# Kernel optimization log

Hardware: AMD Instinct MI355X
Metric: run time of the kernel (lower is better)

## Reference

```python
import jax, jax.numpy as jnp
import numpy as np

B, N, D, F = 4096, 64, 64, 4096
KP_DIM = N * (N + 1) // 2  # 2080
# static row-major triu/tril index lists (matches torch.masked_select ordering)
_TRIU_I, _TRIU_J = (np.array(a) for a in np.triu_indices(N, 0))
_TRIL_I, _TRIL_J = (np.array(a) for a in np.tril_indices(N, 0))


def setup_inputs() -> dict:
    key = jax.random.key(0)
    k1, k2, k3, k4 = jax.random.split(key, 4)
    feature_emb = jax.random.normal(k1, (B, N, D), dtype=jnp.float32)
    # xavier_normal for [D, D]
    std = float(np.sqrt(2.0 / (D + D)))
    kp_W = jax.random.normal(k2, (D, D), dtype=jnp.float32) * std
    # nn.Linear weights are [out_features, in_features]
    bound = float(1.0 / np.sqrt(KP_DIM))
    W_triu = jax.random.uniform(k3, (F, KP_DIM), dtype=jnp.float32, minval=-bound, maxval=bound)
    W_tril = jax.random.uniform(k4, (F, KP_DIM), dtype=jnp.float32, minval=-bound, maxval=bound)
    return {"feature_emb": feature_emb, "kp_W": kp_W, "W_triu": W_triu, "W_tril": W_tril}


def reference(feature_emb, kp_W, W_triu, W_tril):
    # embs_kp[b,i,j] = e[b,i,:] @ kp_W @ e[b,j,:]  -> [B, N, N]
    embs_kp = jnp.einsum("bnd,de,bme->bnm", feature_emb, kp_W, feature_emb)
    triu = embs_kp[:, _TRIU_I, _TRIU_J]  # [B, kp_dim], row-major order
    tril = embs_kp[:, _TRIL_I, _TRIL_J]  # [B, kp_dim]
    embs_flatten = feature_emb.reshape(feature_emb.shape[0], -1)  # [B, N*D]
    view_1 = triu @ W_triu.T  # [B, F]
    view_2 = tril @ W_tril.T  # [B, F]
    return (embs_flatten, view_1, view_2)
```

## Files before the change

### kernel.cpp

```cpp
#include <hip/hip_runtime.h>

typedef __bf16 bf16x8 __attribute__((ext_vector_type(8)));
typedef float f32x4 __attribute__((ext_vector_type(4)));
typedef unsigned short u16x4 __attribute__((ext_vector_type(4)));
typedef unsigned short u16x8 __attribute__((ext_vector_type(8)));

#define KP 2112
#define NT 33

__device__ __forceinline__ unsigned short f2bf(float f) {
  unsigned int u = __builtin_bit_cast(unsigned int, f);
  u += 0x7FFFu + ((u >> 16) & 1u);
  return (unsigned short)(u >> 16);
}

__device__ __forceinline__ bf16x8 ld_frag(const unsigned short* p) {
  return __builtin_bit_cast(bf16x8, *(const u16x8*)p);
}

#define MFMA16(a, b, c) __builtin_amdgcn_mfma_f32_16x16x32_bf16((a), (b), (c), 0, 0, 0)

__device__ __forceinline__ void cp16(const void* g, void* l) {
  __builtin_amdgcn_global_load_lds(
      (const __attribute__((address_space(1))) unsigned int*)g,
      (__attribute__((address_space(3))) unsigned int*)l, 16, 0, 0);
}

__device__ __forceinline__ void barrier_sync() {
  asm volatile("s_waitcnt lgkmcnt(0)" ::: "memory");
  __builtin_amdgcn_s_barrier();
  __builtin_amdgcn_sched_barrier(0);
}

#define VMWAIT(N) asm volatile("s_waitcnt vmcnt(" #N ")" ::: "memory")

__global__ __launch_bounds__(256) void cvt_pad(
    const float* __restrict__ inu, const float* __restrict__ inl,
    unsigned short* __restrict__ outu, unsigned short* __restrict__ outl) {
  const float* in = blockIdx.y ? inl : inu;
  unsigned short* out = blockIdx.y ? outl : outu;
  const int row = blockIdx.x;
  const float* src = in + (size_t)row * 2080;
  unsigned short* dst = out + (size_t)row * KP;
  for (int c = threadIdx.x; c < 528; c += 256) {
    u16x4 o = {0, 0, 0, 0};
    if (c < 520) {
      float4 v = *(const float4*)(src + c * 4);
      o[0] = f2bf(v.x); o[1] = f2bf(v.y); o[2] = f2bf(v.z); o[3] = f2bf(v.w);
    }
    ((u16x4*)dst)[c] = o;
  }
}

__global__ __launch_bounds__(256) void prep_wt(const float* __restrict__ W,
                                               unsigned short* __restrict__ Wt) {
  const int o = blockIdx.x * 256 + threadIdx.x;
  const int c = o >> 6, d = o & 63;
  Wt[o] = f2bf(W[d * 64 + c]);
}

__device__ __forceinline__ void emit_tri(const unsigned short* __restrict__ sK,
                                         unsigned short* __restrict__ dst,
                                         bool upper, int tid) {
#pragma unroll
  for (int jj = 0; jj < 2; ++jj) {
    if (jj == 1 && tid >= 8) break;
    const int p0 = (jj == 0) ? tid * 8 : 2048 + tid * 8;
    int i, j;
    if (upper) {
      float s = sqrtf(4160.25f - 2.0f * (float)p0);
      i = (int)(64.5f - s);
      if (i < 0) i = 0;
      if (i > 63) i = 63;
      while (i > 0 && i * (129 - i) / 2 > p0) --i;
      while (i < 63 && (i + 1) * (128 - i) / 2 <= p0) ++i;
      j = i + (p0 - i * (129 - i) / 2);
    } else {
      float s = sqrtf(8.0f * (float)p0 + 1.0f);
      i = (int)((s - 1.0f) * 0.5f);
      if (i < 0) i = 0;
      if (i > 63) i = 63;
      while (i > 0 && i * (i + 1) / 2 > p0) --i;
      while (i < 63 && (i + 1) * (i + 2) / 2 <= p0) ++i;
      j = p0 - i * (i + 1) / 2;
    }
    u16x8 o;
#pragma unroll
    for (int e = 0; e < 8; ++e) {
      const int p = p0 + e;
      o[e] = (p < 2080 && i < 64) ? sK[i * 64 + j] : (unsigned short)0;
      if (upper) { if (++j > 63) { ++i; j = i; } }
      else       { if (++j > i)  { ++i; j = 0; } }
    }
    *(u16x8*)(dst + p0) = o;
  }
}

__global__ __launch_bounds__(256) void batch_kp(
    const float* __restrict__ E,
    const unsigned short* __restrict__ Wt,
    float* __restrict__ out0,
    unsigned short* __restrict__ triu,
    unsigned short* __restrict__ tril)
{
  __shared__ __align__(16) unsigned short sE[64 * 64];
  __shared__ __align__(16) unsigned short sWt[64 * 64];
  __shared__ __align__(16) unsigned short sT[64 * 64];

  const int b = blockIdx.x;
  const int tid = threadIdx.x;
  const float* Eb = E + (size_t)b * 4096;
  float* o0 = out0 + (size_t)b * 4096;

  cp16(Wt + tid * 8, sWt + tid * 8);
  cp16(Wt + 2048 + tid * 8, sWt + 2048 + tid * 8);

#pragma unroll
  for (int it = 0; it < 4; ++it) {
    const int flat = it * 1024 + tid * 4;
    float4 v = *(const float4*)(Eb + flat);
    *(float4*)(o0 + flat) = v;
    u16x4 e;
    e[0] = f2bf(v.x); e[1] = f2bf(v.y); e[2] = f2bf(v.z); e[3] = f2bf(v.w);
    *(u16x4*)(sE + flat) = e;
  }
  __syncthreads();

  const int lane = tid & 63, w = tid >> 6;
  const int fr = lane & 15;
  const int fk = (lane >> 4) << 3;
  const int qr = (lane >> 4) << 2;

#pragma unroll
  for (int ct = 0; ct < 4; ++ct) {
    f32x4 acc = {0.f, 0.f, 0.f, 0.f};
#pragma unroll
    for (int k2 = 0; k2 < 2; ++k2) {
      bf16x8 a = ld_frag(sE + (w * 16 + fr) * 64 + k2 * 32 + fk);
      bf16x8 bb = ld_frag(sWt + (ct * 16 + fr) * 64 + k2 * 32 + fk);
      acc = MFMA16(a, bb, acc);
    }
#pragma unroll
    for (int r = 0; r < 4; ++r)
      sT[(w * 16 + qr + r) * 64 + ct * 16 + fr] = f2bf(acc[r]);
  }
  __syncthreads();

  unsigned short* sK = sWt;
#pragma unroll
  for (int ct = 0; ct < 4; ++ct) {
    f32x4 acc = {0.f, 0.f, 0.f, 0.f};
#pragma unroll
    for (int k2 = 0; k2 < 2; ++k2) {
      bf16x8 a = ld_frag(sT + (w * 16 + fr) * 64 + k2 * 32 + fk);
      bf16x8 bb = ld_frag(sE + (ct * 16 + fr) * 64 + k2 * 32 + fk);
      acc = MFMA16(a, bb, acc);
    }
#pragma unroll
    for (int r = 0; r < 4; ++r)
      sK[(w * 16 + qr + r) * 64 + ct * 16 + fr] = f2bf(acc[r]);
  }
  __syncthreads();

  emit_tri(sK, triu + (size_t)b * KP, true, tid);
  emit_tri(sK, tril + (size_t)b * KP, false, tid);
}

__global__ __launch_bounds__(512, 2) void gemm_views(
    const unsigned short* __restrict__ triu, const unsigned short* __restrict__ tril,
    const unsigned short* __restrict__ Wu, const unsigned short* __restrict__ Wl,
    float* __restrict__ dout)
{
  __shared__ __align__(16) unsigned short lds[65536];

  const int z = blockIdx.z;
  const unsigned short* Ag = z ? tril : triu;
  const unsigned short* Bg = z ? Wl : Wu;
  float* C = dout + (size_t)16777216 * (size_t)(1 + z);

  const int tid = threadIdx.x;
  const int lane = tid & 63, wv = tid >> 6;
  const int m0 = blockIdx.y << 8, n0 = blockIdx.x << 8;

  const int lr = lane >> 3;
  const int cuch = (lane & 7) ^ lr;
  const int rA = wv * 8 + lr;
  const int rB = (wv & 3) * 8 + (wv >> 2) * 64 + lr;
  const unsigned short* gA = Ag + (size_t)(m0 + rA) * KP + cuch * 8;
  const unsigned short* gB = Bg + (size_t)(n0 + rB) * KP + cuch * 8;
  const int dA = tid * 8;
  const int dB = (wv & 3) * 512 + (wv >> 2) * 4096 + lane * 8;

  const int fr = lane & 15, fq = lane >> 4;
  const int rowA0 = (wv >> 2) * 128 + fr;
  const int rowB0 = (wv & 3) * 64 + fr;

  f32x4 acc[8][4] = {};
  bf16x8 aA_[4], aB_[4], bA_[4], bB_[4];

#define STAGE_A(B_, KT, OFF) do { \
    cp16(gA + (size_t)(OFF) * KP + (KT) * 64, lds + (B_) * 32768 + (OFF) * 64 + dA); \
    cp16(gA + (size_t)((OFF) + 128) * KP + (KT) * 64, \
         lds + (B_) * 32768 + ((OFF) + 128) * 64 + dA); \
  } while (0)
#define STAGE_B(B_, KT, OFF) do { \
    cp16(gB + (size_t)(OFF) * KP + (KT) * 64, \
         lds + (B_) * 32768 + 16384 + (OFF) * 64 + dB); \
    cp16(gB + (size_t)((OFF) + 128) * KP + (KT) * 64, \
         lds + (B_) * 32768 + 16384 + ((OFF) + 128) * 64 + dB); \
  } while (0)
#define LDA(S, B_, MH, KH) do { _Pragma("unroll") \
    for (int mt = 0; mt < 4; ++mt) \
      S[mt] = ld_frag(lds + (B_) * 32768 + (rowA0 + (MH) * 64 + mt * 16) * 64 + \
                      ((((KH) * 4 + fq) ^ (fr & 7)) * 8)); \
  } while (0)
#define LDB(S, B_, KH) do { _Pragma("unroll") \
    for (int nt = 0; nt < 4; ++nt) \
      S[nt] = ld_frag(lds + (B_) * 32768 + 16384 + (rowB0 + nt * 16) * 64 + \
                      ((((KH) * 4 + fq) ^ (fr & 7)) * 8)); \
  } while (0)
#define PH_MFMA(AS, BS, MH) do { \
    __builtin_amdgcn_s_setprio(1); \
    _Pragma("unroll") for (int mt = 0; mt < 4; ++mt) \
    _Pragma("unroll") for (int nt = 0; nt < 4; ++nt) \
      acc[(MH) * 4 + mt][nt] = MFMA16(AS[mt], BS[nt], acc[(MH) * 4 + mt][nt]); \
    __builtin_amdgcn_s_setprio(0); \
  } while (0)

  STAGE_A(0, 0, 0);
  STAGE_B(0, 0, 0);
  STAGE_B(0, 0, 32);
  STAGE_A(0, 0, 64);
  STAGE_B(1, 1, 0);
  STAGE_B(1, 1, 32);
  STAGE_A(1, 1, 0);
  VMWAIT(6);
  barrier_sync();
  LDA(aB_, 0, 0, 0);
  LDB(bA_, 0, 0);

  for (int t = 0; t < NT; ++t) {
    const int cb = t & 1, nb = cb ^ 1;
    const int t1 = (t + 1 < NT) ? t + 1 : NT - 1;
    const int t2 = (t + 2 < NT) ? t + 2 : NT - 1;
    LDA(aA_, cb, 1, 0);
    STAGE_A(nb, t1, 64);
    PH_MFMA(aB_, bA_, 0);
    barrier_sync();
    LDA(aB_, cb, 1, 1);
    LDB(bB_, cb, 1);
    PH_MFMA(aA_, bA_, 1);
    barrier_sync();
    LDA(aA_, cb, 0, 1);
    STAGE_B(cb, t2, 0);
    PH_MFMA(aB_, bB_, 1);
    VMWAIT(4);
    barrier_sync();
    LDA(aB_, nb, 0, 0);
    LDB(bA_, nb, 0);
    STAGE_B(cb, t2, 32);
    STAGE_A(cb, t2, 0);
    PH_MFMA(aA_, bB_, 0);
    VMWAIT(6);
    barrier_sync();
  }

  const int qr = fq << 2;
  const int crow = m0 + (wv >> 2) * 128 + qr;
  const int ccol = n0 + (wv & 3) * 64 + fr;
#pragma unroll
  for (int mt = 0; mt < 8; ++mt)
#pragma unroll
    for (int nt = 0; nt < 4; ++nt) {
      float* cp = C + (size_t)(crow + mt * 16) * 4096 + (ccol + nt * 16);
#pragma unroll
      for (int r = 0; r < 4; ++r) cp[(size_t)r * 4096] = acc[mt][nt][r];
    }
#undef STAGE_A
#undef STAGE_B
#undef LDA
#undef LDB
#undef PH_MFMA
}

extern "C" void kernel_launch(void* const* d_in, const int* in_sizes, int n_in,
                              void* d_out, int out_size, void* d_ws, size_t ws_size,
                              hipStream_t stream) {
  const float* feat  = (const float*)d_in[0];
  const float* kpW   = (const float*)d_in[1];
  const float* Wtriu = (const float*)d_in[2];
  const float* Wtril = (const float*)d_in[3];
  float* out = (float*)d_out;

  const size_t per = (size_t)4096 * KP;
  unsigned short* triu_bf = (unsigned short*)d_ws;
  unsigned short* tril_bf = triu_bf + per;
  unsigned short* Wu_bf   = tril_bf + per;
  unsigned short* Wl_bf   = Wu_bf + per;
  unsigned short* Wt_bf   = Wl_bf + per;

  cvt_pad<<<dim3(4096, 2), dim3(256), 0, stream>>>(Wtriu, Wtril, Wu_bf, Wl_bf);
  prep_wt<<<dim3(16), dim3(256), 0, stream>>>(kpW, Wt_bf);
  batch_kp<<<dim3(4096), dim3(256), 0, stream>>>(feat, Wt_bf, out, triu_bf, tril_bf);
  gemm_views<<<dim3(16, 16, 2), dim3(512), 0, stream>>>(triu_bf, tril_bf, Wu_bf, Wl_bf, out);
}
```

Before: 428.4 us.

## Fuse prep kernels into one launch and restructure GEMM barrier pipeline

Merges the weight fp32->bf16 conversion, the kp_W transpose, and the per-batch bilinear kernel into a single launch. Extra blocks handle the weight conversion and each batch block transposes kp_W itself, which removes two kernel launches and the Wt workspace round trip. The GEMM main loop is also rescheduled: LDS fragment loads now sit before a barrier that waits on lgkmcnt, with a separate closing barrier, rather than being prefetched across phases. This trades some register-level load/MFMA overlap for fewer live fragment registers, and adds redundant kp_W reads plus scattered LDS stores in every batch block.

```diff
diff --git a/kernel.cpp b/kernel.cpp
--- a/kernel.cpp
+++ b/kernel.cpp
@@ -26,38 +26,18 @@
       (__attribute__((address_space(3))) unsigned int*)l, 16, 0, 0);
 }
 
-__device__ __forceinline__ void barrier_sync() {
+__device__ __forceinline__ void gate() {
+  __builtin_amdgcn_s_barrier();
   asm volatile("s_waitcnt lgkmcnt(0)" ::: "memory");
+  __builtin_amdgcn_sched_barrier(0);
+}
+__device__ __forceinline__ void close_bar() {
+  asm volatile("" ::: "memory");
   __builtin_amdgcn_s_barrier();
   __builtin_amdgcn_sched_barrier(0);
 }
 
 #define VMWAIT(N) asm volatile("s_waitcnt vmcnt(" #N ")" ::: "memory")
-
-__global__ __launch_bounds__(256) void cvt_pad(
-    const float* __restrict__ inu, const float* __restrict__ inl,
-    unsigned short* __restrict__ outu, unsigned short* __restrict__ outl) {
-  const float* in = blockIdx.y ? inl : inu;
-  unsigned short* out = blockIdx.y ? outl : outu;
-  const int row = blockIdx.x;
-  const float* src = in + (size_t)row * 2080;
-  unsigned short* dst = out + (size_t)row * KP;
-  for (int c = threadIdx.x; c < 528; c += 256) {
-    u16x4 o = {0, 0, 0, 0};
-    if (c < 520) {
-      float4 v = *(const float4*)(src + c * 4);
-      o[0] = f2bf(v.x); o[1] = f2bf(v.y); o[2] = f2bf(v.z); o[3] = f2bf(v.w);
-    }
-    ((u16x4*)dst)[c] = o;
-  }
-}
-
-__global__ __launch_bounds__(256) void prep_wt(const float* __restrict__ W,
-                                               unsigned short* __restrict__ Wt) {
-  const int o = blockIdx.x * 256 + threadIdx.x;
-  const int c = o >> 6, d = o & 63;
-  Wt[o] = f2bf(W[d * 64 + c]);
-}
 
 __device__ __forceinline__ void emit_tri(const unsigned short* __restrict__ sK,
                                          unsigned short* __restrict__ dst,
@@ -96,24 +76,46 @@
   }
 }
 
-__global__ __launch_bounds__(256) void batch_kp(
+__global__ __launch_bounds__(256) void prep_all(
     const float* __restrict__ E,
-    const unsigned short* __restrict__ Wt,
+    const float* __restrict__ Wkp,
+    const float* __restrict__ Wtriu,
+    const float* __restrict__ Wtril,
     float* __restrict__ out0,
     unsigned short* __restrict__ triu,
-    unsigned short* __restrict__ tril)
+    unsigned short* __restrict__ tril,
+    unsigned short* __restrict__ Wu,
+    unsigned short* __restrict__ Wl)
 {
+  const int bid = blockIdx.x;
+  const int tid = threadIdx.x;
+
+  if (bid >= 4096) {
+    const int r0 = (bid - 4096) * 2;
+#pragma unroll
+    for (int q = 0; q < 4; ++q) {
+      const int row = r0 + (q & 1);
+      const float* src = (q < 2 ? Wtriu : Wtril) + (size_t)row * 2080;
+      unsigned short* dst = (q < 2 ? Wu : Wl) + (size_t)row * KP;
+      for (int c = tid; c < 528; c += 256) {
+        u16x4 o = {0, 0, 0, 0};
+        if (c < 520) {
+          float4 v = *(const float4*)(src + c * 4);
+          o[0] = f2bf(v.x); o[1] = f2bf(v.y); o[2] = f2bf(v.z); o[3] = f2bf(v.w);
+        }
+        ((u16x4*)dst)[c] = o;
+      }
+    }
+    return;
+  }
+
   __shared__ __align__(16) unsigned short sE[64 * 64];
   __shared__ __align__(16) unsigned short sWt[64 * 64];
   __shared__ __align__(16) unsigned short sT[64 * 64];
 
-  const int b = blockIdx.x;
-  const int tid = threadIdx.x;
+  const int b = bid;
   const float* Eb = E + (size_t)b * 4096;
   float* o0 = out0 + (size_t)b * 4096;
-
-  cp16(Wt + tid * 8, sWt + tid * 8);
-  cp16(Wt + 2048 + tid * 8, sWt + 2048 + tid * 8);
 
 #pragma unroll
   for (int it = 0; it < 4; ++it) {
@@ -123,6 +125,12 @@
     u16x4 e;
     e[0] = f2bf(v.x); e[1] = f2bf(v.y); e[2] = f2bf(v.z); e[3] = f2bf(v.w);
     *(u16x4*)(sE + flat) = e;
+    float4 wv = *(const float4*)(Wkp + flat);
+    const int d = flat >> 6, c0 = flat & 63;
+    sWt[(c0 + 0) * 64 + d] = f2bf(wv.x);
+    sWt[(c0 + 1) * 64 + d] = f2bf(wv.y);
+    sWt[(c0 + 2) * 64 + d] = f2bf(wv.z);
+    sWt[(c0 + 3) * 64 + d] = f2bf(wv.w);
   }
   __syncthreads();
 
@@ -196,7 +204,7 @@
   const int rowB0 = (wv & 3) * 64 + fr;
 
   f32x4 acc[8][4] = {};
-  bf16x8 aA_[4], aB_[4], bA_[4], bB_[4];
+  bf16x8 a_[4], aX_[4], b0_[4], b1_[4];
 
 #define STAGE_A(B_, KT, OFF) do { \
     cp16(gA + (size_t)(OFF) * KP + (KT) * 64, lds + (B_) * 32768 + (OFF) * 64 + dA); \
@@ -235,34 +243,36 @@
   STAGE_B(1, 1, 32);
   STAGE_A(1, 1, 0);
   VMWAIT(6);
-  barrier_sync();
-  LDA(aB_, 0, 0, 0);
-  LDB(bA_, 0, 0);
+  close_bar();
 
   for (int t = 0; t < NT; ++t) {
     const int cb = t & 1, nb = cb ^ 1;
     const int t1 = (t + 1 < NT) ? t + 1 : NT - 1;
     const int t2 = (t + 2 < NT) ? t + 2 : NT - 1;
-    LDA(aA_, cb, 1, 0);
+    LDA(a_, cb, 0, 0);
+    LDB(b0_, cb, 0);
     STAGE_A(nb, t1, 64);
-    PH_MFMA(aB_, bA_, 0);
-    barrier_sync();
-    LDA(aB_, cb, 1, 1);
-    LDB(bB_, cb, 1);
-    PH_MFMA(aA_, bA_, 1);
-    barrier_sync();
-    LDA(aA_, cb, 0, 1);
+    gate();
+    PH_MFMA(a_, b0_, 0);
+    close_bar();
+    LDA(a_, cb, 1, 0);
+    LDB(b1_, cb, 1);
+    gate();
+    PH_MFMA(a_, b0_, 1);
+    close_bar();
+    LDA(a_, cb, 1, 1);
+    LDA(aX_, cb, 0, 1);
     STAGE_B(cb, t2, 0);
-    PH_MFMA(aB_, bB_, 1);
+    gate();
+    PH_MFMA(a_, b1_, 1);
     VMWAIT(4);
-    barrier_sync();
-    LDA(aB_, nb, 0, 0);
-    LDB(bA_, nb, 0);
+    close_bar();
     STAGE_B(cb, t2, 32);
     STAGE_A(cb, t2, 0);
-    PH_MFMA(aA_, bB_, 0);
+    gate();
+    PH_MFMA(aX_, b1_, 0);
     VMWAIT(6);
-    barrier_sync();
+    close_bar();
   }
 
   const int qr = fq << 2;
@@ -297,10 +307,8 @@
   unsigned short* tril_bf = triu_bf + per;
   unsigned short* Wu_bf   = tril_bf + per;
   unsigned short* Wl_bf   = Wu_bf + per;
-  unsigned short* Wt_bf   = Wl_bf + per;
-
-  cvt_pad<<<dim3(4096, 2), dim3(256), 0, stream>>>(Wtriu, Wtril, Wu_bf, Wl_bf);
-  prep_wt<<<dim3(16), dim3(256), 0, stream>>>(kpW, Wt_bf);
-  batch_kp<<<dim3(4096), dim3(256), 0, stream>>>(feat, Wt_bf, out, triu_bf, tril_bf);
+
+  prep_all<<<dim3(6144), dim3(256), 0, stream>>>(
+      feat, kpW, Wtriu, Wtril, out, triu_bf, tril_bf, Wu_bf, Wl_bf);
   gemm_views<<<dim3(16, 16, 2), dim3(512), 0, stream>>>(triu_bf, tril_bf, Wu_bf, Wl_bf, out);
 }
```

After: 424.0 us. About the same (-1.0%).
